# Optimization experiments

Measured on AMD Instinct MI355X. Metric: run time of the kernel, lower is better.

The kernel has to match this reference:

```python
import jax, jax.numpy as jnp
import numpy as np

B = 1024          # number of graphs (subjects)
N1_PER = 116      # nodes per graph, branch 1 (AAL atlas)
N2_PER = 200      # nodes per graph, branch 2 (CC200 atlas)
DEG = 16          # sparsified adjacency degree
H = 32            # hidden_dim
NUM_CLASSES = 2


def _make_graph(key, b, n, deg):
    """Block-diagonal sparse adjacency in COO form, deg edges per node within its block."""
    N = b * n
    E = N * deg
    rows = jnp.repeat(jnp.arange(N, dtype=jnp.int32), deg)
    offs = jax.random.randint(jax.random.fold_in(key, 0), (E,), 0, n, dtype=jnp.int32)
    cols = (rows // n) * n + offs
    vals = jax.random.uniform(jax.random.fold_in(key, 1), (E,), dtype=jnp.float32)
    return rows, cols, vals


def setup_inputs() -> dict:
    key = jax.random.key(0)
    ks = jax.random.split(key, 20)
    rows1, cols1, vals1 = _make_graph(ks[0], B, N1_PER, DEG)
    rows2, cols2, vals2 = _make_graph(ks[1], B, N2_PER, DEG)
    x1 = jax.random.normal(ks[2], (B * N1_PER, N1_PER), dtype=jnp.float32)
    x2 = jax.random.normal(ks[3], (B * N2_PER, N2_PER), dtype=jnp.float32)
    s = 0.1
    inp = {
        "rows1": rows1, "cols1": cols1, "vals1": vals1, "x1": x1,
        "rows2": rows2, "cols2": cols2, "vals2": vals2, "x2": x2,
        # GCN branch 116
        "W1a": jax.random.normal(ks[4], (N1_PER, H), dtype=jnp.float32) * s,
        "b1a": jnp.zeros((H,), jnp.float32),
        "W1b": jax.random.normal(ks[5], (H, H), dtype=jnp.float32) * s,
        "b1b": jnp.zeros((H,), jnp.float32),
        # GCN branch 200
        "W2a": jax.random.normal(ks[6], (N2_PER, H), dtype=jnp.float32) * s,
        "b2a": jnp.zeros((H,), jnp.float32),
        "W2b": jax.random.normal(ks[7], (H, H), dtype=jnp.float32) * s,
        "b2b": jnp.zeros((H,), jnp.float32),
        # MLP head (stored as (in, out))
        "fc1_W": jax.random.normal(ks[8], (4 * H, H), dtype=jnp.float32) * s,
        "fc1_b": jnp.zeros((H,), jnp.float32),
        "fc2_W": jax.random.normal(ks[9], (H, H // 2), dtype=jnp.float32) * s,
        "fc2_b": jnp.zeros((H // 2,), jnp.float32),
        "fc3_W": jax.random.normal(ks[10], (H // 2, NUM_CLASSES), dtype=jnp.float32) * s,
        "fc3_b": jnp.zeros((NUM_CLASSES,), jnp.float32),
    }
    return inp


def _gcn(rows, cols, vals, x, W, b):
    # support = X @ W  (dense GEMM), then sparse aggregation A @ support, then bias
    support = x @ W                              # [N, H]
    msg = vals[:, None] * support[cols]          # gather + scale, [E, H]
    agg = jax.ops.segment_sum(msg, rows, num_segments=x.shape[0])  # scatter-add
    return agg + b


def _branch(rows, cols, vals, x, Wa, ba, Wb, bb, n_per):
    h = jax.nn.relu(_gcn(rows, cols, vals, x, Wa, ba))
    h = jax.nn.relu(_gcn(rows, cols, vals, h, Wb, bb))
    h = h.reshape(-1, n_per, h.shape[-1])        # [B, n, H]
    return jnp.concatenate([h.mean(axis=1), h.max(axis=1)], axis=1)  # [B, 2H]


def reference(rows1, cols1, vals1, x1, rows2, cols2, vals2, x2,
              W1a, b1a, W1b, b1b, W2a, b2a, W2b, b2b,
              fc1_W, fc1_b, fc2_W, fc2_b, fc3_W, fc3_b):
    f116 = _branch(rows1, cols1, vals1, x1, W1a, b1a, W1b, b1b, N1_PER)
    f200 = _branch(rows2, cols2, vals2, x2, W2a, b2a, W2b, b2b, N2_PER)
    x = jnp.concatenate([f116, f200], axis=1)    # [B, 4H]
    h = jax.nn.relu(x @ fc1_W + fc1_b)           # dropout is identity at inference
    h = jax.nn.relu(h @ fc2_W + fc2_b)
    logits = h @ fc3_W + fc3_b                   # [B, 2]
    return logits
```

## Files before the change

### kernel.cpp

```cpp
#include <hip/hip_runtime.h>

#define NB 1024
#define N1P 116
#define N2P 200
#define HD 32


__device__ __forceinline__ void agg_phase(int base, int NPv,
                                          const int* __restrict__ cols,
                                          const float* __restrict__ vals,
                                          const float* __restrict__ sup,
                                          float bias, float* __restrict__ outh,
                                          int tid) {
    const int h = tid & 31;
    for (int n = tid >> 5; n < NPv; n += 8) {
        const int4* c4 = (const int4*)(cols + ((size_t)base + n) * 16);
        const float4* v4 = (const float4*)(vals + ((size_t)base + n) * 16);
        float a = bias;
#pragma unroll
        for (int q = 0; q < 4; ++q) {
            const int4 c = c4[q];
            const float4 v = v4[q];
            a += v.x * sup[(c.x - base) * 32 + h];
            a += v.y * sup[(c.y - base) * 32 + h];
            a += v.z * sup[(c.z - base) * 32 + h];
            a += v.w * sup[(c.w - base) * 32 + h];
        }
        outh[n * 32 + h] = fmaxf(a, 0.f);
    }
}

template <int NK>
__device__ __forceinline__ void row_gemm_acc(float* acc, const float* __restrict__ xrow,
                                             const float* __restrict__ W) {
#pragma unroll 1
    for (int k4 = 0; k4 < NK; k4 += 4) {
        const float4 x4 = *(const float4*)&xrow[k4];
#pragma unroll
        for (int kk = 0; kk < 4; ++kk) {
            const float xs = (&x4.x)[kk];
            const float* w = W + (k4 + kk) * 32;
#pragma unroll
            for (int c4 = 0; c4 < 8; ++c4) {
                const float4 wv = *(const float4*)&w[c4 * 4];
                acc[c4 * 4 + 0] += xs * wv.x;
                acc[c4 * 4 + 1] += xs * wv.y;
                acc[c4 * 4 + 2] += xs * wv.z;
                acc[c4 * 4 + 3] += xs * wv.w;
            }
        }
    }
}

template <int NP>
__device__ void branch_graph(int g,
                             const float* __restrict__ X,
                             const int* __restrict__ cols,
                             const float* __restrict__ vals,
                             const float* __restrict__ Wa,
                             const float* __restrict__ ba,
                             const float* __restrict__ Wb,
                             const float* __restrict__ bb,
                             float* __restrict__ feats, int foff,
                             float* sSup, float* sH) {
    const int tid = threadIdx.x;
    const int base = g * NP;
    const float* xg = X + (size_t)base * NP;
    const float bA = ba[tid & 31];
    const float bB = bb[tid & 31];

    constexpr int KC = 16;
    constexpr int SXS = 20;
    float* sX = sSup;
    float acc[32];
#pragma unroll
    for (int c = 0; c < 32; ++c) acc[c] = 0.f;

    const int NC = (NP + KC - 1) / KC;
#pragma unroll 1
    for (int kc = 0; kc < NC; ++kc) {
        const int k0 = kc * KC;
        const int kw = (NP - k0) < KC ? (NP - k0) : KC;
        const int pieces = kw >> 2;
        for (int i = tid; i < NP * 4; i += 256) {
            const int row = i >> 2, p = i & 3;
            if (p < pieces) {
                const float4 v = *(const float4*)(xg + (size_t)row * NP + k0 + p * 4);
                *(float4*)&sX[row * SXS + p * 4] = v;
            }
        }
        __syncthreads();
        if (tid < NP) {
            const float* wbase = Wa + k0 * 32;
            const float* xrow = &sX[tid * SXS];
#pragma unroll 1
            for (int k4 = 0; k4 < kw; k4 += 4) {
                const float4 x4 = *(const float4*)&xrow[k4];
#pragma unroll
                for (int kk = 0; kk < 4; ++kk) {
                    const float xs = (&x4.x)[kk];
                    const float* w = wbase + (k4 + kk) * 32;
#pragma unroll
                    for (int c4 = 0; c4 < 8; ++c4) {
                        const float4 wv = *(const float4*)&w[c4 * 4];
                        acc[c4 * 4 + 0] += xs * wv.x;
                        acc[c4 * 4 + 1] += xs * wv.y;
                        acc[c4 * 4 + 2] += xs * wv.z;
                        acc[c4 * 4 + 3] += xs * wv.w;
                    }
                }
            }
        }
        __syncthreads();
    }
    if (tid < NP) {
#pragma unroll
        for (int c4 = 0; c4 < 8; ++c4) {
            float4 o;
            o.x = acc[c4 * 4 + 0]; o.y = acc[c4 * 4 + 1];
            o.z = acc[c4 * 4 + 2]; o.w = acc[c4 * 4 + 3];
            *(float4*)&sSup[tid * 32 + c4 * 4] = o;
        }
    }
    __syncthreads();

    agg_phase(base, NP, cols, vals, sSup, bA, sH, tid);
    __syncthreads();

    if (tid < NP) {
        float acc2[32];
#pragma unroll
        for (int c = 0; c < 32; ++c) acc2[c] = 0.f;
        row_gemm_acc<32>(acc2, &sH[tid * 32], Wb);
#pragma unroll
        for (int c4 = 0; c4 < 8; ++c4) {
            float4 o;
            o.x = acc2[c4 * 4 + 0]; o.y = acc2[c4 * 4 + 1];
            o.z = acc2[c4 * 4 + 2]; o.w = acc2[c4 * 4 + 3];
            *(float4*)&sSup[tid * 32 + c4 * 4] = o;
        }
    }
    __syncthreads();

    agg_phase(base, NP, cols, vals, sSup, bB, sH, tid);
    __syncthreads();

    const int h = tid & 31, sl = tid >> 5;
    float sum = 0.f, mx = -1e30f;
    for (int n = sl; n < NP; n += 8) {
        const float v = sH[n * 32 + h];
        sum += v;
        mx = fmaxf(mx, v);
    }
    float* sS = sSup;
    float* sM = sSup + 256;
    sS[tid] = sum;
    sM[tid] = mx;
    __syncthreads();
    if (tid < 32) {
#pragma unroll
        for (int q = 1; q < 8; ++q) {
            sum += sS[tid + 32 * q];
            mx = fmaxf(mx, sM[tid + 32 * q]);
        }
        feats[(size_t)g * 128 + foff + tid] = sum * (1.0f / NP);
        feats[(size_t)g * 128 + foff + 32 + tid] = mx;
    }
}

__global__ __launch_bounds__(256, 2) void fused_branches(
        const float* __restrict__ x1, const int* __restrict__ cols1,
        const float* __restrict__ vals1,
        const float* __restrict__ W1a, const float* __restrict__ b1a,
        const float* __restrict__ W1b, const float* __restrict__ b1b,
        const float* __restrict__ x2, const int* __restrict__ cols2,
        const float* __restrict__ vals2,
        const float* __restrict__ W2a, const float* __restrict__ b2a,
        const float* __restrict__ W2b, const float* __restrict__ b2b,
        float* __restrict__ feats) {
    __shared__ float sSup[N2P * 32];
    __shared__ float sH[N2P * 32];
    const int bid = blockIdx.x;
    if (bid < NB) {
        branch_graph<N1P>(bid, x1, cols1, vals1, W1a, b1a, W1b, b1b, feats, 0,
                          sSup, sH);
    } else {
        branch_graph<N2P>(bid - NB, x2, cols2, vals2, W2a, b2a, W2b, b2b, feats,
                          64, sSup, sH);
    }
}

__global__ __launch_bounds__(256) void mlp_head(const float* __restrict__ feats,
                                                const float* __restrict__ W1,
                                                const float* __restrict__ b1,
                                                const float* __restrict__ W2,
                                                const float* __restrict__ b2,
                                                const float* __restrict__ W3,
                                                const float* __restrict__ b3,
                                                float* __restrict__ out) {
    __shared__ float sW1[128 * 32];
    __shared__ float sW2[32 * 16];
    __shared__ float sW3[16 * 2];
    __shared__ float sB1[32], sB2[16], sB3[2];
    __shared__ float sF[8 * 128];
    __shared__ float sH1[8 * 32];
    __shared__ float sH2[8 * 16];

    const int tid = threadIdx.x;
    for (int idx = tid; idx < 128 * 32; idx += 256) sW1[idx] = W1[idx];
    for (int idx = tid; idx < 32 * 16; idx += 256) sW2[idx] = W2[idx];
    if (tid < 32) { sW3[tid] = W3[tid]; sB1[tid] = b1[tid]; }
    if (tid < 16) sB2[tid] = b2[tid];
    if (tid < 2) sB3[tid] = b3[tid];
    const long g0 = (long)blockIdx.x * 8;
    for (int idx = tid; idx < 1024; idx += 256) sF[idx] = feats[g0 * 128 + idx];
    __syncthreads();

    const int g = tid >> 5, h = tid & 31;
    float a1 = sB1[h];
#pragma unroll 4
    for (int k = 0; k < 128; ++k) a1 += sF[g * 128 + k] * sW1[k * 32 + h];
    sH1[g * 32 + h] = fmaxf(a1, 0.f);
    __syncthreads();

    if (h < 16) {
        float a2 = sB2[h];
#pragma unroll
        for (int k = 0; k < 32; ++k) a2 += sH1[g * 32 + k] * sW2[k * 16 + h];
        sH2[g * 16 + h] = fmaxf(a2, 0.f);
    }
    __syncthreads();

    if (h < 2) {
        float a3 = sB3[h];
#pragma unroll
        for (int k = 0; k < 16; ++k) a3 += sH2[g * 16 + k] * sW3[k * 2 + h];
        out[(g0 + g) * 2 + h] = a3;
    }
}

extern "C" void kernel_launch(void* const* d_in, const int* in_sizes, int n_in,
                              void* d_out, int out_size, void* d_ws, size_t ws_size,
                              hipStream_t stream) {
    const int*   cols1 = (const int*)d_in[1];
    const float* vals1 = (const float*)d_in[2];
    const float* x1    = (const float*)d_in[3];
    const int*   cols2 = (const int*)d_in[5];
    const float* vals2 = (const float*)d_in[6];
    const float* x2    = (const float*)d_in[7];
    const float* W1a = (const float*)d_in[8];
    const float* b1a = (const float*)d_in[9];
    const float* W1b = (const float*)d_in[10];
    const float* b1b = (const float*)d_in[11];
    const float* W2a = (const float*)d_in[12];
    const float* b2a = (const float*)d_in[13];
    const float* W2b = (const float*)d_in[14];
    const float* b2b = (const float*)d_in[15];
    const float* fc1_W = (const float*)d_in[16];
    const float* fc1_b = (const float*)d_in[17];
    const float* fc2_W = (const float*)d_in[18];
    const float* fc2_b = (const float*)d_in[19];
    const float* fc3_W = (const float*)d_in[20];
    const float* fc3_b = (const float*)d_in[21];
    float* out = (float*)d_out;

    float* feats = (float*)d_ws;

    fused_branches<<<2 * NB, 256, 0, stream>>>(
        x1, cols1, vals1, W1a, b1a, W1b, b1b,
        x2, cols2, vals2, W2a, b2a, W2b, b2b, feats);

    mlp_head<<<NB / 8, 256, 0, stream>>>(feats, fc1_W, fc1_b, fc2_W, fc2_b,
                                         fc3_W, fc3_b, out);
}
```

Before: 535.9 us.

## Prefetch X chunks into registers, pad shared stride to 33, raise occupancy

The first-layer GEMM now loads the next 16-column chunk of X into registers while the current chunk is being computed, so global load latency overlaps with compute. The shared-memory row stride for support and hidden buffers goes from 32 to 33 floats to reduce LDS bank conflicts. The launch bound asks for 3 blocks per CU instead of 2. The padded stride makes the float4 LDS accesses unaligned, which may split or slow those accesses. The extra prefetch registers add register pressure against the tighter occupancy target.

Measured after the change: 493.9 us. -7.8%, faster.

```diff
diff --git a/kernel.cpp b/kernel.cpp
--- a/kernel.cpp
+++ b/kernel.cpp
@@ -6,6 +6,7 @@
 #define HD 32
 
 
+template <int ST>
 __device__ __forceinline__ void agg_phase(int base, int NPv,
                                           const int* __restrict__ cols,
                                           const float* __restrict__ vals,
@@ -21,34 +22,12 @@
         for (int q = 0; q < 4; ++q) {
             const int4 c = c4[q];
             const float4 v = v4[q];
-            a += v.x * sup[(c.x - base) * 32 + h];
-            a += v.y * sup[(c.y - base) * 32 + h];
-            a += v.z * sup[(c.z - base) * 32 + h];
-            a += v.w * sup[(c.w - base) * 32 + h];
-        }
-        outh[n * 32 + h] = fmaxf(a, 0.f);
-    }
-}
-
-template <int NK>
-__device__ __forceinline__ void row_gemm_acc(float* acc, const float* __restrict__ xrow,
-                                             const float* __restrict__ W) {
-#pragma unroll 1
-    for (int k4 = 0; k4 < NK; k4 += 4) {
-        const float4 x4 = *(const float4*)&xrow[k4];
-#pragma unroll
-        for (int kk = 0; kk < 4; ++kk) {
-            const float xs = (&x4.x)[kk];
-            const float* w = W + (k4 + kk) * 32;
-#pragma unroll
-            for (int c4 = 0; c4 < 8; ++c4) {
-                const float4 wv = *(const float4*)&w[c4 * 4];
-                acc[c4 * 4 + 0] += xs * wv.x;
-                acc[c4 * 4 + 1] += xs * wv.y;
-                acc[c4 * 4 + 2] += xs * wv.z;
-                acc[c4 * 4 + 3] += xs * wv.w;
-            }
-        }
+            a += v.x * sup[(c.x - base) * ST + h];
+            a += v.y * sup[(c.y - base) * ST + h];
+            a += v.z * sup[(c.z - base) * ST + h];
+            a += v.w * sup[(c.w - base) * ST + h];
+        }
+        outh[n * ST + h] = fmaxf(a, 0.f);
     }
 }
 
@@ -63,43 +42,74 @@
                              const float* __restrict__ bb,
                              float* __restrict__ feats, int foff,
                              float* sSup, float* sH) {
+    constexpr int ST = 33;
+    constexpr int KC = 16;
+    constexpr int SXS = 20;
+    constexpr int NSLOT = NP * 4;
+    constexpr int PSL = (NSLOT + 255) / 256;
+
     const int tid = threadIdx.x;
     const int base = g * NP;
     const float* xg = X + (size_t)base * NP;
     const float bA = ba[tid & 31];
     const float bB = bb[tid & 31];
 
-    constexpr int KC = 16;
-    constexpr int SXS = 20;
     float* sX = sSup;
+
     float acc[32];
 #pragma unroll
     for (int c = 0; c < 32; ++c) acc[c] = 0.f;
 
     const int NC = (NP + KC - 1) / KC;
-#pragma unroll 1
-    for (int kc = 0; kc < NC; ++kc) {
+
+    float4 cur[PSL], nxt[PSL];
+
+    auto load_chunk = [&](int kc, float4* buf) {
         const int k0 = kc * KC;
         const int kw = (NP - k0) < KC ? (NP - k0) : KC;
         const int pieces = kw >> 2;
-        for (int i = tid; i < NP * 4; i += 256) {
-            const int row = i >> 2, p = i & 3;
-            if (p < pieces) {
-                const float4 v = *(const float4*)(xg + (size_t)row * NP + k0 + p * 4);
-                *(float4*)&sX[row * SXS + p * 4] = v;
+#pragma unroll
+        for (int q = 0; q < PSL; ++q) {
+            const int i = tid + q * 256;
+            float4 v = make_float4(0.f, 0.f, 0.f, 0.f);
+            if (i < NSLOT) {
+                const int row = i >> 2, p = i & 3;
+                if (p < pieces)
+                    v = *(const float4*)(xg + (size_t)row * NP + k0 + p * 4);
             }
-        }
+            buf[q] = v;
+        }
+    };
+    auto store_chunk = [&](const float4* buf) {
+#pragma unroll
+        for (int q = 0; q < PSL; ++q) {
+            const int i = tid + q * 256;
+            if (i < NSLOT) {
+                const int row = i >> 2, p = i & 3;
+                *(float4*)&sX[row * SXS + p * 4] = buf[q];
+            }
+        }
+    };
+
+    load_chunk(0, cur);
+#pragma unroll 1
+    for (int kc = 0; kc < NC; ++kc) {
         __syncthreads();
+        store_chunk(cur);
+        __syncthreads();
+        if (kc + 1 < NC) load_chunk(kc + 1, nxt);
+        const int k0 = kc * KC;
+        const int kw = (NP - k0) < KC ? (NP - k0) : KC;
         if (tid < NP) {
-            const float* wbase = Wa + k0 * 32;
             const float* xrow = &sX[tid * SXS];
+            const float* wb0 = Wa + (size_t)k0 * 32;
 #pragma unroll 1
             for (int k4 = 0; k4 < kw; k4 += 4) {
                 const float4 x4 = *(const float4*)&xrow[k4];
 #pragma unroll
                 for (int kk = 0; kk < 4; ++kk) {
                     const float xs = (&x4.x)[kk];
-                    const float* w = wbase + (k4 + kk) * 32;
+                    const float* w = wb0 + (k4 + kk) * 32;
 #pragma unroll
                     for (int c4 = 0; c4 < 8; ++c4) {
                         const float4 wv = *(const float4*)&w[c4 * 4];
@@ -111,44 +121,64 @@
                 }
             }
         }
-        __syncthreads();
-    }
+#pragma unroll
+        for (int q = 0; q < PSL; ++q) cur[q] = nxt[q];
+    }
+    __syncthreads();
+
     if (tid < NP) {
 #pragma unroll
         for (int c4 = 0; c4 < 8; ++c4) {
             float4 o;
             o.x = acc[c4 * 4 + 0]; o.y = acc[c4 * 4 + 1];
             o.z = acc[c4 * 4 + 2]; o.w = acc[c4 * 4 + 3];
-            *(float4*)&sSup[tid * 32 + c4 * 4] = o;
-        }
-    }
-    __syncthreads();
-
-    agg_phase(base, NP, cols, vals, sSup, bA, sH, tid);
+            *(float4*)&sSup[tid * ST + c4 * 4] = o;
+        }
+    }
+    __syncthreads();
+
+    agg_phase<ST>(base, NP, cols, vals, sSup, bA, sH, tid);
     __syncthreads();
 
     if (tid < NP) {
         float acc2[32];
 #pragma unroll
         for (int c = 0; c < 32; ++c) acc2[c] = 0.f;
-        row_gemm_acc<32>(acc2, &sH[tid * 32], Wb);
+        const float* xrow = &sH[tid * ST];
+#pragma unroll 1
+        for (int k4 = 0; k4 < 32; k4 += 4) {
+            const float4 x4 = *(const float4*)&xrow[k4];
+#pragma unroll
+            for (int kk = 0; kk < 4; ++kk) {
+                const float xs = (&x4.x)[kk];
+                const float* w = Wb + (k4 + kk) * 32;
+#pragma unroll
+                for (int c4 = 0; c4 < 8; ++c4) {
+                    const float4 wv = *(const float4*)&w[c4 * 4];
+                    acc2[c4 * 4 + 0] += xs * wv.x;
+                    acc2[c4 * 4 + 1] += xs * wv.y;
+                    acc2[c4 * 4 + 2] += xs * wv.z;
+                    acc2[c4 * 4 + 3] += xs * wv.w;
+                }
+            }
+        }
 #pragma unroll
         for (int c4 = 0; c4 < 8; ++c4) {
             float4 o;
             o.x = acc2[c4 * 4 + 0]; o.y = acc2[c4 * 4 + 1];
             o.z = acc2[c4 * 4 + 2]; o.w = acc2[c4 * 4 + 3];
-            *(float4*)&sSup[tid * 32 + c4 * 4] = o;
-        }
-    }
-    __syncthreads();
-
-    agg_phase(base, NP, cols, vals, sSup, bB, sH, tid);
+            *(float4*)&sSup[tid * ST + c4 * 4] = o;
+        }
+    }
+    __syncthreads();
+
+    agg_phase<ST>(base, NP, cols, vals, sSup, bB, sH, tid);
     __syncthreads();
 
     const int h = tid & 31, sl = tid >> 5;
     float sum = 0.f, mx = -1e30f;
     for (int n = sl; n < NP; n += 8) {
-        const float v = sH[n * 32 + h];
+        const float v = sH[n * ST + h];
         sum += v;
         mx = fmaxf(mx, v);
     }
@@ -168,7 +198,7 @@
     }
 }
 
-__global__ __launch_bounds__(256, 2) void fused_branches(
+__global__ __launch_bounds__(256, 3) void fused_branches(
         const float* __restrict__ x1, const int* __restrict__ cols1,
         const float* __restrict__ vals1,
         const float* __restrict__ W1a, const float* __restrict__ b1a,
@@ -178,8 +208,8 @@
         const float* __restrict__ W2a, const float* __restrict__ b2a,
         const float* __restrict__ W2b, const float* __restrict__ b2b,
         float* __restrict__ feats) {
-    __shared__ float sSup[N2P * 32];
-    __shared__ float sH[N2P * 32];
+    __shared__ float sSup[N2P * 33];
+    __shared__ float sH[N2P * 33];
     const int bid = blockIdx.x;
     if (bid < NB) {
         branch_graph<N1P>(bid, x1, cols1, vals1, W1a, b1a, W1b, b1b, feats, 0,
```
